# Kernel optimization log

Measured on AMD Instinct MI355X. Metric: run time of the kernel, lower is better.

Reference implementation:

```python
import jax, jax.numpy as jnp
import numpy as np

S, B, E, H = 2048, 2, 1024, 16
D = E // H


def setup_inputs() -> dict:
    key = jax.random.key(0)
    k1, k2, k3, k4 = jax.random.split(key, 4)
    x = jax.random.normal(k1, (S, B, E), dtype=jnp.float32)
    # xavier_uniform for [3E, E] and [O, E]
    lim_qkv = float(np.sqrt(6.0 / (3 * E + E)))
    lim_out = float(np.sqrt(6.0 / (E + E)))
    w_qkv = jax.random.uniform(k2, (3 * E, E), jnp.float32, -lim_qkv, lim_qkv)
    b_qkv = jnp.zeros((3 * E,), jnp.float32)
    w_out = jax.random.uniform(k3, (E, E), jnp.float32, -lim_out, lim_out)
    b_out = jnp.zeros((E,), jnp.float32)
    return {"x": x, "w_qkv": w_qkv, "b_qkv": b_qkv, "w_out": w_out, "b_out": b_out}


def reference(x, w_qkv, b_qkv, w_out, b_out):
    # x: [S, B, E] (seq-first, as in the torch module)
    s, b, e = x.shape
    scaling = jnp.asarray(np.sqrt(D), x.dtype)
    qkv = jnp.einsum('sbe,fe->sbf', x, w_qkv) + b_qkv          # [S,B,3E]
    q, k, v = jnp.split(qkv, 3, axis=-1)
    q = q.reshape(s, b, H, D)
    k = k.reshape(s, b, H, D)
    v = v.reshape(s, b, H, D)
    # scores [B,H,S,S]; note original divides by sqrt(head_dim)
    scores = jnp.einsum('sbhd,tbhd->bhst', q, k) / scaling
    attn_w = jax.nn.softmax(scores.astype(jnp.float32), axis=-1).astype(scores.dtype)
    # dropout p=0.1 is identity in eval mode (training=False)
    attn = jnp.einsum('bhst,tbhd->sbhd', attn_w, v).reshape(s, b, e)
    out = jnp.einsum('sbe,oe->sbo', attn, w_out) + b_out        # [S,B,O]
    attn_avg = attn_w.mean(axis=1)                              # [B,S,S]
    return out, attn_avg
```

## Files before the change

### kernel.cpp

```cpp
#include <hip/hip_runtime.h>

#define SEQ   2048
#define BATCH 2
#define NH    16
#define HD    64
#define EMB   1024

#define QSCALE 0.18033688011112042f

using bf16x8 = __attribute__((ext_vector_type(8))) short;
using f32x4  = __attribute__((ext_vector_type(4))) float;
using f32x16 = __attribute__((ext_vector_type(16))) float;

__device__ __forceinline__ unsigned short f2bf(float f) {
  unsigned int u = __float_as_uint(f);
  u += 0x7FFFu + ((u >> 16) & 1u);
  return (unsigned short)(u >> 16);
}
__device__ __forceinline__ unsigned pk_bf16(float lo, float hi) {
  unsigned r;
  asm("v_cvt_pk_bf16_f32 %0, %1, %2" : "=v"(r) : "v"(lo), "v"(hi));
  return r;
}
__device__ __forceinline__ void gload16(const void* g, void* l) {
  __builtin_amdgcn_global_load_lds(
      (const __attribute__((address_space(1))) unsigned int*)g,
      (__attribute__((address_space(3))) unsigned int*)l, 16, 0, 0);
}

__global__ __launch_bounds__(256) void cvt_f32_bf16(const float* __restrict__ in,
                                                    unsigned short* __restrict__ out,
                                                    int n4) {
  int i = blockIdx.x * 256 + threadIdx.x;
  if (i < n4) {
    float4 v = reinterpret_cast<const float4*>(in)[i];
    ushort4 o;
    o.x = f2bf(v.x); o.y = f2bf(v.y); o.z = f2bf(v.z); o.w = f2bf(v.w);
    reinterpret_cast<ushort4*>(out)[i] = o;
  }
}

template <int EPI>
__global__ __launch_bounds__(256) void gemm_bt(
    const unsigned short* __restrict__ A,
    const unsigned short* __restrict__ B,
    const float* __restrict__ bias,
    float* __restrict__ Cf,
    unsigned short* __restrict__ Qb,
    unsigned short* __restrict__ Kb,
    unsigned short* __restrict__ VTb,
    int M, int N, int K) {
  __shared__ int4 As[128][8];
  __shared__ int4 Bs[128][8];
  const int tid = threadIdx.x;
  const int wid = tid >> 6, lane = tid & 63;
  const int wm = wid >> 1, wn = wid & 1;
  const int lg = lane >> 4, lr = lane & 15;
  const int lr8 = lane >> 3;
  const int lc8 = (lane & 7) ^ lr8;
  const int row0 = blockIdx.x * 128, col0 = blockIdx.y * 128;
  f32x4 acc[4][4] = {};
  for (int k0 = 0; k0 < K; k0 += 64) {
#pragma unroll
    for (int i = 0; i < 4; i++) {
      const int rb = wid * 32 + i * 8;
      gload16(&A[(size_t)(row0 + rb + lr8) * K + k0 + lc8 * 8], &As[rb][0]);
      gload16(&B[(size_t)(col0 + rb + lr8) * K + k0 + lc8 * 8], &Bs[rb][0]);
    }
    __syncthreads();
#pragma unroll
    for (int ks = 0; ks < 2; ks++) {
      bf16x8 af[4], bfr[4];
#pragma unroll
      for (int mi = 0; mi < 4; mi++) {
        int r = wm * 64 + mi * 16 + lr;
        af[mi] = *reinterpret_cast<const bf16x8*>(&As[r][(ks * 4 + lg) ^ (r & 7)]);
      }
#pragma unroll
      for (int ni = 0; ni < 4; ni++) {
        int r = wn * 64 + ni * 16 + lr;
        bfr[ni] = *reinterpret_cast<const bf16x8*>(&Bs[r][(ks * 4 + lg) ^ (r & 7)]);
      }
#pragma unroll
      for (int mi = 0; mi < 4; mi++)
#pragma unroll
        for (int ni = 0; ni < 4; ni++)
          acc[mi][ni] = __builtin_amdgcn_mfma_f32_16x16x32_bf16(af[mi], bfr[ni], acc[mi][ni], 0, 0, 0);
    }
    __syncthreads();
  }
#pragma unroll
  for (int mi = 0; mi < 4; mi++)
#pragma unroll
    for (int ni = 0; ni < 4; ni++) {
      const int row_b = row0 + wm * 64 + mi * 16 + lg * 4;
      const int col = col0 + wn * 64 + ni * 16 + lr;
      const float bs = bias[col];
      float v0 = acc[mi][ni][0] + bs;
      float v1 = acc[mi][ni][1] + bs;
      float v2 = acc[mi][ni][2] + bs;
      float v3 = acc[mi][ni][3] + bs;
      if (EPI == 0) {
        Cf[(size_t)(row_b + 0) * N + col] = v0;
        Cf[(size_t)(row_b + 1) * N + col] = v1;
        Cf[(size_t)(row_b + 2) * N + col] = v2;
        Cf[(size_t)(row_b + 3) * N + col] = v3;
      } else {
        const int which = col >> 10, rr = col & 1023;
        const int hh = rr >> 6, d = rr & 63;
        if (which == 2) {
          const int s0 = row_b >> 1;
          ushort2 p0; p0.x = f2bf(v0); p0.y = f2bf(v2);
          ushort2 p1; p1.x = f2bf(v1); p1.y = f2bf(v3);
          *reinterpret_cast<ushort2*>(&VTb[((size_t)((0 * NH + hh) * HD + d)) * SEQ + s0]) = p0;
          *reinterpret_cast<ushort2*>(&VTb[((size_t)((1 * NH + hh) * HD + d)) * SEQ + s0]) = p1;
        } else {
          unsigned short* dst = which == 0 ? Qb : Kb;
          const float sc = (which == 0) ? QSCALE : 1.0f;
          float vv[4] = {v0 * sc, v1 * sc, v2 * sc, v3 * sc};
#pragma unroll
          for (int r = 0; r < 4; r++) {
            int s = (row_b + r) >> 1, bb = r & 1;
            dst[(size_t)((bb * NH + hh) * SEQ + s) * HD + d] = f2bf(vv[r]);
          }
        }
      }
    }
}

__global__ __launch_bounds__(256, 2) void attn1(
    const unsigned short* __restrict__ Qb,
    const unsigned short* __restrict__ Kb,
    const unsigned short* __restrict__ VTb,
    unsigned short* __restrict__ attn_bf,
    float* __restrict__ lbuf) {
  __shared__ int4 Kt[2][64][8];
  __shared__ int4 Vt[2][64][8];
  const int tid = threadIdx.x;
  const int wid = tid >> 6, lane = tid & 63;
  const int l31 = lane & 31, lhi = lane >> 5;
  const int lr8 = lane >> 3;
  const int lc8 = (lane & 7) ^ lr8;
  const int L = blockIdx.x;
  const int v = (L & 7) * 64 + (L >> 3);
  const int bh = v >> 4, stile = v & 15;
  const int b = bh >> 4, h = bh & 15;
  const int s0 = stile * 128 + wid * 32;
  const unsigned short* Qg = Qb + (size_t)bh * SEQ * HD;
  const unsigned short* Kg = Kb + (size_t)bh * SEQ * HD;
  const unsigned short* VTg = VTb + (size_t)bh * HD * SEQ;

  bf16x8 qf[4];
#pragma unroll
  for (int ks = 0; ks < 4; ks++)
    qf[ks] = *reinterpret_cast<const bf16x8*>(Qg + (size_t)(s0 + l31) * HD + ks * 16 + lhi * 8);

  auto stage = [&](int tg, int buf) {
#pragma unroll
    for (int i = 0; i < 2; i++) {
      const int rb = wid * 16 + i * 8;
      gload16(Kg + (size_t)(tg * 64 + rb + lr8) * HD + lc8 * 8, &Kt[buf][rb][0]);
      gload16(VTg + (size_t)(rb + lr8) * SEQ + tg * 64 + lc8 * 8, &Vt[buf][rb][0]);
    }
  };

  stage(0, 0);
  __syncthreads();

  f32x16 o[2] = {};
  float ls = 0.f;

  for (int t = 0; t < 32; t++) {
    const int cur = t & 1;
    if (t + 1 < 32) stage(t + 1, cur ^ 1);
    f32x16 st[2] = {};
    __builtin_amdgcn_s_setprio(1);
#pragma unroll
    for (int ks = 0; ks < 4; ks++)
#pragma unroll
      for (int ti = 0; ti < 2; ti++) {
        const int row = ti * 32 + l31;
        bf16x8 kf = *reinterpret_cast<const bf16x8*>(&Kt[cur][row][(ks * 2 + lhi) ^ (row & 7)]);
        st[ti] = __builtin_amdgcn_mfma_f32_32x32x16_bf16(kf, qf[ks], st[ti], 0, 0, 0);
      }
    __builtin_amdgcn_s_setprio(0);
    bf16x8 vf[2][4];
#pragma unroll
    for (int dt = 0; dt < 2; dt++)
#pragma unroll
      for (int c = 0; c < 4; c++) {
        const int row = dt * 32 + l31;
        vf[dt][c] = *reinterpret_cast<const bf16x8*>(&Vt[cur][row][(c * 2 + lhi) ^ (row & 7)]);
      }
    float p[32];
    float psum = 0.f;
#pragma unroll
    for (int ti = 0; ti < 2; ti++)
#pragma unroll
      for (int r = 0; r < 16; r++) {
        float e = __builtin_amdgcn_exp2f(st[ti][r]);
        p[ti * 16 + r] = e;
        psum += e;
      }
    ls += psum;
#pragma unroll
    for (int c = 0; c < 4; c++) {
      const int ti = c >> 1, cc = c & 1;
      const int pb = ti * 16 + cc * 8;
      unsigned w0 = pk_bf16(p[pb + 0], p[pb + 1]);
      unsigned w1 = pk_bf16(p[pb + 2], p[pb + 3]);
      unsigned w2 = pk_bf16(p[pb + 4], p[pb + 5]);
      unsigned w3 = pk_bf16(p[pb + 6], p[pb + 7]);
      asm volatile("v_permlane32_swap_b32 %0, %1" : "+v"(w0), "+v"(w2));
      asm volatile("v_permlane32_swap_b32 %0, %1" : "+v"(w1), "+v"(w3));
      union { unsigned u[4]; bf16x8 v; } pa;
      pa.u[0] = w0;
      pa.u[1] = w1;
      pa.u[2] = w2;
      pa.u[3] = w3;
      __builtin_amdgcn_s_setprio(1);
#pragma unroll
      for (int dt = 0; dt < 2; dt++)
        o[dt] = __builtin_amdgcn_mfma_f32_32x32x16_bf16(pa.v, vf[dt][c], o[dt], 0, 0, 0);
      __builtin_amdgcn_s_setprio(0);
    }
    __syncthreads();
  }

  ls += __shfl_xor(ls, 32, 64);
  if (lhi == 0)
    lbuf[(size_t)bh * SEQ + s0 + l31] = ls;

#pragma unroll
  for (int r = 0; r < 16; r++) {
    const int s_off = (r & 3) + 8 * (r >> 2) + 4 * lhi;
    float denom = __shfl(ls, s_off, 64);
    float inv = __builtin_amdgcn_rcpf(denom);
    const int s = s0 + s_off;
#pragma unroll
    for (int dt = 0; dt < 2; dt++) {
      float ov = o[dt][r] * inv;
      attn_bf[((size_t)s * BATCH + b) * EMB + h * HD + dt * 32 + l31] = f2bf(ov);
    }
  }
}

__global__ __launch_bounds__(256) void attn2(
    const unsigned short* __restrict__ Qb,
    const unsigned short* __restrict__ Kb,
    const float* __restrict__ lbuf,
    float* __restrict__ avg_out) {
  const int b = blockIdx.z;
  const int s0 = blockIdx.y * 64;
  const int tc0 = blockIdx.x * 256;
  __shared__ int4 Qs[64][8];
  __shared__ int4 Ks[2][64][8];
  __shared__ float lls[NH][64];
  const int tid = threadIdx.x;
  const int wid = tid >> 6, lane = tid & 63;
  const int wm = wid >> 1, wn = wid & 1;
  const int lg = lane >> 4, lr = lane & 15;
  const int lr8 = lane >> 3;
  const int lc8 = (lane & 7) ^ lr8;

  for (int i = tid; i < NH * 64; i += 256) {
    int hh = i >> 6, r = i & 63;
    lls[hh][r] = 1.0f / ((float)NH * lbuf[(b * NH + hh) * SEQ + s0 + r]);
  }

  const size_t bh0 = (size_t)(b * NH) * SEQ;

  auto stageK = [&](const unsigned short* src, int buf) {
#pragma unroll
    for (int i = 0; i < 2; i++) {
      const int rb = wid * 16 + i * 8;
      gload16(src + (size_t)(rb + lr8) * HD + lc8 * 8, &Ks[buf][rb][0]);
    }
  };
  auto stageQ = [&](const unsigned short* src) {
#pragma unroll
    for (int i = 0; i < 2; i++) {
      const int rb = wid * 16 + i * 8;
      gload16(src + (size_t)(rb + lr8) * HD + lc8 * 8, &Qs[rb][0]);
    }
  };

  stageQ(Qb + (bh0 + s0) * HD);
  stageK(Kb + (bh0 + tc0) * HD, 0);
  __syncthreads();

  f32x4 avg[4][2][2] = {};

  for (int h = 0; h < NH; h++) {
    bf16x8 af[2][2];
#pragma unroll
    for (int mi = 0; mi < 2; mi++) {
      int r = wm * 32 + mi * 16 + lr;
#pragma unroll
      for (int ks = 0; ks < 2; ks++)
        af[mi][ks] = *reinterpret_cast<const bf16x8*>(&Qs[r][(ks * 4 + lg) ^ (r & 7)]);
    }
    float linv[2][4];
#pragma unroll
    for (int mi = 0; mi < 2; mi++)
#pragma unroll
      for (int r = 0; r < 4; r++)
        linv[mi][r] = lls[h][wm * 32 + mi * 16 + lg * 4 + r];

    const unsigned short* Kgh = Kb + (bh0 + (size_t)h * SEQ + tc0) * HD;

    for (int t0 = 0; t0 < 4; t0++) {
      const int cur = t0 & 1;
      if (t0 < 3) {
        stageK(Kgh + (size_t)(t0 + 1) * 64 * HD, cur ^ 1);
      } else if (h + 1 < NH) {
        stageK(Kb + (bh0 + (size_t)(h + 1) * SEQ + tc0) * HD, cur ^ 1);
        stageQ(Qb + (bh0 + (size_t)(h + 1) * SEQ + s0) * HD);
      }
      f32x4 sacc[2][2] = {};
      __builtin_amdgcn_s_setprio(1);
#pragma unroll
      for (int ks = 0; ks < 2; ks++) {
        bf16x8 bk[2];
#pragma unroll
        for (int ni = 0; ni < 2; ni++) {
          int rk = wn * 32 + ni * 16 + lr;
          bk[ni] = *reinterpret_cast<const bf16x8*>(&Ks[cur][rk][(ks * 4 + lg) ^ (rk & 7)]);
        }
#pragma unroll
        for (int mi = 0; mi < 2; mi++)
#pragma unroll
          for (int ni = 0; ni < 2; ni++)
            sacc[mi][ni] = __builtin_amdgcn_mfma_f32_16x16x32_bf16(af[mi][ks], bk[ni], sacc[mi][ni], 0, 0, 0);
      }
      __builtin_amdgcn_s_setprio(0);
#pragma unroll
      for (int mi = 0; mi < 2; mi++)
#pragma unroll
        for (int ni = 0; ni < 2; ni++)
#pragma unroll
          for (int r = 0; r < 4; r++)
            avg[t0][mi][ni][r] += __builtin_amdgcn_exp2f(sacc[mi][ni][r]) * linv[mi][r];
      __syncthreads();
    }
  }

#pragma unroll
  for (int t0 = 0; t0 < 4; t0++)
#pragma unroll
    for (int mi = 0; mi < 2; mi++)
#pragma unroll
      for (int ni = 0; ni < 2; ni++)
#pragma unroll
        for (int r = 0; r < 4; r++) {
          int s = s0 + wm * 32 + mi * 16 + lg * 4 + r;
          int t = tc0 + t0 * 64 + wn * 32 + ni * 16 + lr;
          avg_out[((size_t)b * SEQ + s) * SEQ + t] = avg[t0][mi][ni][r];
        }
}

extern "C" void kernel_launch(void* const* d_in, const int* in_sizes, int n_in,
                              void* d_out, int out_size, void* d_ws, size_t ws_size,
                              hipStream_t stream) {
  const float* x     = (const float*)d_in[0];
  const float* w_qkv = (const float*)d_in[1];
  const float* b_qkv = (const float*)d_in[2];
  const float* w_out = (const float*)d_in[3];
  const float* b_out = (const float*)d_in[4];
  float* out = (float*)d_out;
  float* avg = out + (size_t)SEQ * BATCH * EMB;

  char* ws = (char*)d_ws;
  size_t off = 0;
  unsigned short* x_bf    = (unsigned short*)(ws + off); off += (size_t)SEQ * BATCH * EMB * 2;
  unsigned short* wqkv_bf = (unsigned short*)(ws + off); off += (size_t)3 * EMB * EMB * 2;
  unsigned short* wout_bf = (unsigned short*)(ws + off); off += (size_t)EMB * EMB * 2;
  unsigned short* Qbuf    = (unsigned short*)(ws + off); off += (size_t)BATCH * NH * SEQ * HD * 2;
  unsigned short* Kbuf    = (unsigned short*)(ws + off); off += (size_t)BATCH * NH * SEQ * HD * 2;
  unsigned short* VTbuf   = (unsigned short*)(ws + off); off += (size_t)BATCH * NH * HD * SEQ * 2;
  unsigned short* attn_bf = (unsigned short*)(ws + off); off += (size_t)SEQ * BATCH * EMB * 2;
  float*          lbuf    = (float*)(ws + off);          off += (size_t)BATCH * NH * SEQ * 4;

  cvt_f32_bf16<<<(SEQ * BATCH * EMB / 4) / 256, 256, 0, stream>>>(x, x_bf, SEQ * BATCH * EMB / 4);
  cvt_f32_bf16<<<(3 * EMB * EMB / 4) / 256, 256, 0, stream>>>(w_qkv, wqkv_bf, 3 * EMB * EMB / 4);
  cvt_f32_bf16<<<(EMB * EMB / 4) / 256, 256, 0, stream>>>(w_out, wout_bf, EMB * EMB / 4);

  gemm_bt<1><<<dim3(SEQ * BATCH / 128, 3 * EMB / 128), 256, 0, stream>>>(
      x_bf, wqkv_bf, b_qkv, nullptr, Qbuf, Kbuf, VTbuf, SEQ * BATCH, 3 * EMB, EMB);

  attn1<<<512, 256, 0, stream>>>(Qbuf, Kbuf, VTbuf, attn_bf, lbuf);

  attn2<<<dim3(SEQ / 256, SEQ / 64, BATCH), 256, 0, stream>>>(Qbuf, Kbuf, lbuf, avg);

  gemm_bt<0><<<dim3(SEQ * BATCH / 128, EMB / 128), 256, 0, stream>>>(
      attn_bf, wout_bf, b_out, out, nullptr, nullptr, nullptr, SEQ * BATCH, EMB, EMB);
}
```

Before: 153.0 us.

## Software-pipeline attention loop so PV MFMAs of previous tile overlap QK and softmax

Restructures the flash-attention inner loop so that the P·V MFMAs for tile t-1 are issued together with the QK MFMAs for tile t, with the exp/pack softmax and V fragment loads deferred to the end of each iteration, plus a prologue and epilogue. The goal is to let the matrix units run while the exp and pack VALU work proceeds, instead of alternating in strict dependency order. It also seeds the first MFMA of each accumulation with a zero constant rather than zero-initialising accumulators, in both the attention and the averaged-weights kernels. The cost is more live registers (packed P and V fragments held across iterations), which can lower occupancy or cause spills.

```diff
diff --git a/kernel.cpp b/kernel.cpp
--- a/kernel.cpp
+++ b/kernel.cpp
@@ -164,34 +164,29 @@
     }
   };
 
-  stage(0, 0);
-  __syncthreads();
-
+  const f32x16 fz = {};
   f32x16 o[2] = {};
   float ls = 0.f;
-
-  for (int t = 0; t < 32; t++) {
-    const int cur = t & 1;
-    if (t + 1 < 32) stage(t + 1, cur ^ 1);
-    f32x16 st[2] = {};
-    __builtin_amdgcn_s_setprio(1);
-#pragma unroll
-    for (int ks = 0; ks < 4; ks++)
+  bf16x8 paq[4];
+  bf16x8 vfr[2][4];
+
+  auto qk = [&](int cur, f32x16 st[2]) {
+#pragma unroll
+    for (int ti = 0; ti < 2; ti++) {
+      const int row = ti * 32 + l31;
+      bf16x8 kf = *reinterpret_cast<const bf16x8*>(&Kt[cur][row][(lhi) ^ (row & 7)]);
+      st[ti] = __builtin_amdgcn_mfma_f32_32x32x16_bf16(kf, qf[0], fz, 0, 0, 0);
+    }
+#pragma unroll
+    for (int ks = 1; ks < 4; ks++)
 #pragma unroll
       for (int ti = 0; ti < 2; ti++) {
         const int row = ti * 32 + l31;
         bf16x8 kf = *reinterpret_cast<const bf16x8*>(&Kt[cur][row][(ks * 2 + lhi) ^ (row & 7)]);
         st[ti] = __builtin_amdgcn_mfma_f32_32x32x16_bf16(kf, qf[ks], st[ti], 0, 0, 0);
       }
-    __builtin_amdgcn_s_setprio(0);
-    bf16x8 vf[2][4];
-#pragma unroll
-    for (int dt = 0; dt < 2; dt++)
-#pragma unroll
-      for (int c = 0; c < 4; c++) {
-        const int row = dt * 32 + l31;
-        vf[dt][c] = *reinterpret_cast<const bf16x8*>(&Vt[cur][row][(c * 2 + lhi) ^ (row & 7)]);
-      }
+  };
+  auto softpack = [&](const f32x16 st[2]) {
     float p[32];
     float psum = 0.f;
 #pragma unroll
@@ -214,18 +209,55 @@
       asm volatile("v_permlane32_swap_b32 %0, %1" : "+v"(w0), "+v"(w2));
       asm volatile("v_permlane32_swap_b32 %0, %1" : "+v"(w1), "+v"(w3));
       union { unsigned u[4]; bf16x8 v; } pa;
-      pa.u[0] = w0;
-      pa.u[1] = w1;
-      pa.u[2] = w2;
-      pa.u[3] = w3;
-      __builtin_amdgcn_s_setprio(1);
+      pa.u[0] = w0; pa.u[1] = w1; pa.u[2] = w2; pa.u[3] = w3;
+      paq[c] = pa.v;
+    }
+  };
+  auto loadv = [&](int cur) {
+#pragma unroll
+    for (int dt = 0; dt < 2; dt++)
+#pragma unroll
+      for (int c = 0; c < 4; c++) {
+        const int row = dt * 32 + l31;
+        vfr[dt][c] = *reinterpret_cast<const bf16x8*>(&Vt[cur][row][(c * 2 + lhi) ^ (row & 7)]);
+      }
+  };
+
+  stage(0, 0);
+  __syncthreads();
+
+  {
+    stage(1, 1);
+    f32x16 st[2];
+    __builtin_amdgcn_s_setprio(1);
+    qk(0, st);
+    __builtin_amdgcn_s_setprio(0);
+    softpack(st);
+    loadv(0);
+    __syncthreads();
+  }
+
+  for (int t = 1; t < 32; t++) {
+    const int cur = t & 1;
+    if (t + 1 < 32) stage(t + 1, cur ^ 1);
+    f32x16 st[2];
+    __builtin_amdgcn_s_setprio(1);
+#pragma unroll
+    for (int c = 0; c < 4; c++)
 #pragma unroll
       for (int dt = 0; dt < 2; dt++)
-        o[dt] = __builtin_amdgcn_mfma_f32_32x32x16_bf16(pa.v, vf[dt][c], o[dt], 0, 0, 0);
-      __builtin_amdgcn_s_setprio(0);
-    }
+        o[dt] = __builtin_amdgcn_mfma_f32_32x32x16_bf16(paq[c], vfr[dt][c], o[dt], 0, 0, 0);
+    qk(cur, st);
+    __builtin_amdgcn_s_setprio(0);
+    softpack(st);
+    loadv(cur);
     __syncthreads();
   }
+#pragma unroll
+  for (int c = 0; c < 4; c++)
+#pragma unroll
+    for (int dt = 0; dt < 2; dt++)
+      o[dt] = __builtin_amdgcn_mfma_f32_32x32x16_bf16(paq[c], vfr[dt][c], o[dt], 0, 0, 0);
 
   ls += __shfl_xor(ls, 32, 64);
   if (lhi == 0)
@@ -289,6 +321,7 @@
   stageK(Kb + (bh0 + tc0) * HD, 0);
   __syncthreads();
 
+  const f32x4 fz4 = {};
   f32x4 avg[4][2][2] = {};
 
   for (int h = 0; h < NH; h++) {
@@ -317,7 +350,7 @@
         stageK(Kb + (bh0 + (size_t)(h + 1) * SEQ + tc0) * HD, cur ^ 1);
         stageQ(Qb + (bh0 + (size_t)(h + 1) * SEQ + s0) * HD);
       }
-      f32x4 sacc[2][2] = {};
+      f32x4 sacc[2][2];
       __builtin_amdgcn_s_setprio(1);
 #pragma unroll
       for (int ks = 0; ks < 2; ks++) {
@@ -331,7 +364,8 @@
         for (int mi = 0; mi < 2; mi++)
 #pragma unroll
           for (int ni = 0; ni < 2; ni++)
-            sacc[mi][ni] = __builtin_amdgcn_mfma_f32_16x16x32_bf16(af[mi][ks], bk[ni], sacc[mi][ni], 0, 0, 0);
+            sacc[mi][ni] = __builtin_amdgcn_mfma_f32_16x16x32_bf16(
+                af[mi][ks], bk[ni], ks == 0 ? fz4 : sacc[mi][ni], 0, 0, 0);
       }
       __builtin_amdgcn_s_setprio(0);
 #pragma unroll
```

New measurement: 152.9 us. No clear change (-0.1%).
